# Kernel optimization log

Hardware: AMD Instinct MI355X
Metric: run time of the kernel (lower is better)

## Reference

```python
import jax, jax.numpy as jnp
import numpy as np

TEMPERATURE = 0.1
NORMALIZE = True


def setup_inputs() -> dict:
    key = jax.random.key(0)
    k1, k2 = jax.random.split(key)
    B, D = 4096, 512
    return {
        "z_i": jax.random.normal(k1, (B, D), dtype=jnp.float32),
        "z_j": jax.random.normal(k2, (B, D), dtype=jnp.float32),
    }


def _l2norm(x):
    return x / jnp.sqrt(jnp.sum(x * x, axis=-1, keepdims=True))


def reference(z_i, z_j):
    if NORMALIZE:
        z_i = _l2norm(z_i)
        z_j = _l2norm(z_j)
    B = z_i.shape[0]

    inv_t = 1.0 / TEMPERATURE
    logits_aa = (z_i @ z_i.T) * inv_t  # [B, B]
    logits_bb = (z_j @ z_j.T) * inv_t
    logits_ab = (z_i @ z_j.T) * inv_t
    logits_ba = (z_j @ z_i.T) * inv_t

    # Static off-diagonal column indices: row i keeps cols 0..B-1 except i,
    # in ascending order (matches torch boolean-mask row-major extraction).
    j = jnp.arange(B - 1)[None, :]
    i = jnp.arange(B)[:, None]
    idx = j + (j >= i)  # [B, B-1] int32

    take = lambda m: jnp.take_along_axis(m, idx, axis=1)  # [B, B-1]

    pos = jnp.concatenate([jnp.diagonal(logits_ab), jnp.diagonal(logits_ba)])[:, None]  # [2B, 1]
    neg_a = jnp.concatenate([take(logits_aa), take(logits_ab)], axis=1)  # [B, 2(B-1)]
    neg_b = jnp.concatenate([take(logits_ba), take(logits_bb)], axis=1)
    neg = jnp.concatenate([neg_a, neg_b], axis=0)  # [2B, 2(B-1)]

    logits = jnp.concatenate([pos, neg], axis=1)  # [2B, 2B-1]
    logp = jax.nn.log_softmax(logits, axis=1)
    # Original forward uses labels = torch.ones(2B).long() -> target class 1.
    loss = -jnp.mean(logp[:, 1])
    return loss
```

## Files before the change

### kernel.cpp

```cpp
#include <hip/hip_runtime.h>
#include <hip/hip_bf16.h>
#include <hip/hip_fp8.h>


#define BB 4096
#define DD 512
#define NN 8192
#define TILE 128
#define KB 64
#define NBLK 2080

typedef __attribute__((ext_vector_type(4))) float f32x4;

#define AS1 __attribute__((address_space(1)))
#define AS3 __attribute__((address_space(3)))
static __device__ __forceinline__ void gload_lds16(const void* g, void* l) {
    __builtin_amdgcn_global_load_lds((const AS1 void*)g, (AS3 void*)l, 16, 0, 0);
}

__global__ __launch_bounds__(256)
void normalize_kernel(const float* __restrict__ zi, const float* __restrict__ zj,
                      unsigned char* __restrict__ M, float* __restrict__ rowsum) {
    const int wave = threadIdx.x >> 6;
    const int lane = threadIdx.x & 63;
    const int row  = blockIdx.x * 4 + wave;
    if (threadIdx.x < 4) rowsum[blockIdx.x * 4 + threadIdx.x] = 0.f;
    const float* src = (row < BB) ? (zi + (size_t)row * DD)
                                  : (zj + (size_t)(row - BB) * DD);
    float4 v0 = ((const float4*)src)[lane * 2 + 0];
    float4 v1 = ((const float4*)src)[lane * 2 + 1];
    float ss = v0.x*v0.x + v0.y*v0.y + v0.z*v0.z + v0.w*v0.w
             + v1.x*v1.x + v1.y*v1.y + v1.z*v1.z + v1.w*v1.w;
    #pragma unroll
    for (int off = 1; off <= 32; off <<= 1) ss += __shfl_xor(ss, off);
    const float inv = rsqrtf(ss);
    const float vals[8] = {v0.x*inv, v0.y*inv, v0.z*inv, v0.w*inv,
                           v1.x*inv, v1.y*inv, v1.z*inv, v1.w*inv};
    union { long u; unsigned char b[8]; } pk;
    #pragma unroll
    for (int j = 0; j < 8; ++j)
        pk.b[j] = __hip_cvt_float_to_fp8(vals[j], __HIP_SATFINITE, __HIP_E4M3);
    ((long*)(M + (size_t)row * DD))[lane] = pk.u;
}

__global__ __launch_bounds__(256, 4)
void gram_lse_kernel(const unsigned char* __restrict__ Mg,
                     float* __restrict__ rowsum, float* __restrict__ targets) {
    __shared__ __align__(16) char As[2][TILE * KB];
    __shared__ __align__(16) char Bs[2][TILE * KB];

    const int d = blockIdx.x;
    const int p = (d & 7) * 260 + (d >> 3);
    int by = (int)((sqrtf(8.0f * (float)p + 1.0f) - 1.0f) * 0.5f);
    while ((by + 1) * (by + 2) / 2 <= p) ++by;
    while (by * (by + 1) / 2 > p) --by;
    const int bx = p - by * (by + 1) / 2;

    const int rowBase = bx * TILE;
    const int colBase = by * TILE;
    const bool diag = (bx == by);
    const int tid  = threadIdx.x;
    const int wave = tid >> 6;
    const int lane = tid & 63;
    const int wr = (wave >> 1) * 64;
    const int wc = (wave & 1) * 64;
    const int l15 = lane & 15;
    const int l4  = lane >> 4;

    const int sg  = (tid & 3) ^ ((tid >> 3) & 3);
    const int sr0 = tid >> 2;
    const unsigned char* gA0 = Mg + (size_t)(rowBase + sr0) * DD + sg * 16;
    const unsigned char* gB0 = Mg + (size_t)(colBase + sr0) * DD + sg * 16;

    const int r2 = (l15 >> 1) & 3;
    const int qh = l4 >> 1, ql = l4 & 1;
    const int aoff0 = (wr + l15) * KB + ql * 8;
    const int boff0 = (wc + l15) * KB + ql * 8;

    f32x4 acc[4][4] = {};

    {
        char* lA = As[0] + tid * 16;
        #pragma unroll
        for (int i = 0; i < 2; ++i)
            gload_lds16(gA0 + (size_t)i * 64 * DD, lA + i * 4096);
        if (!diag) {
            char* lB = Bs[0] + tid * 16;
            #pragma unroll
            for (int i = 0; i < 2; ++i)
                gload_lds16(gB0 + (size_t)i * 64 * DD, lB + i * 4096);
        }
    }

    #pragma unroll
    for (int t = 0; t < DD / KB; ++t) {
        __syncthreads();
        if (t < DD / KB - 1) {
            const int k0 = (t + 1) * KB;
            char* lA = As[(t + 1) & 1] + tid * 16;
            #pragma unroll
            for (int i = 0; i < 2; ++i)
                gload_lds16(gA0 + k0 + (size_t)i * 64 * DD, lA + i * 4096);
            if (!diag) {
                char* lB = Bs[(t + 1) & 1] + tid * 16;
                #pragma unroll
                for (int i = 0; i < 2; ++i)
                    gload_lds16(gB0 + k0 + (size_t)i * 64 * DD, lB + i * 4096);
            }
        }
        const char* Asrc = As[t & 1];
        const char* Bsrc = diag ? Asrc : Bs[t & 1];
        #pragma unroll
        for (int ks = 0; ks < 2; ++ks) {
            const int so = ((((ks << 1) | qh) ^ r2) << 4);
            long a[4], b[4];
            #pragma unroll
            for (int mi = 0; mi < 4; ++mi)
                a[mi] = *(const long*)(Asrc + aoff0 + mi * 1024 + so);
            #pragma unroll
            for (int ni = 0; ni < 4; ++ni)
                b[ni] = *(const long*)(Bsrc + boff0 + ni * 1024 + so);
            #pragma unroll
            for (int mi = 0; mi < 4; ++mi)
                #pragma unroll
                for (int ni = 0; ni < 4; ++ni)
                    acc[mi][ni] = __builtin_amdgcn_mfma_f32_16x16x32_fp8_fp8(
                        a[mi], b[ni], acc[mi][ni], 0, 0, 0);
        }
    }

    const float C10 = 14.42695040888963f;
    float cs[4] = {0.f, 0.f, 0.f, 0.f};
    #pragma unroll
    for (int mi = 0; mi < 4; ++mi) {
        float rs[4] = {0.f, 0.f, 0.f, 0.f};
        #pragma unroll
        for (int ni = 0; ni < 4; ++ni) {
            const int gcol = colBase + wc + ni * 16 + l15;
            #pragma unroll
            for (int r = 0; r < 4; ++r) {
                const int grow = rowBase + wr + mi * 16 + l4 * 4 + r;
                float e = __builtin_amdgcn_exp2f(fmaf(acc[mi][ni][r], C10, -C10));
                if (grow == gcol) e = 0.f;
                rs[r] += e;
                cs[ni] += e;
                if (rowBase == 0 && grow < 2) {
                    const int j0 = ((gcol & (BB - 1)) == 0) ? 1 : 0;
                    if (grow == j0) targets[gcol] = 10.f * acc[mi][ni][r];
                }
            }
        }
        #pragma unroll
        for (int m = 1; m <= 8; m <<= 1)
            #pragma unroll
            for (int r = 0; r < 4; ++r)
                rs[r] += __shfl_xor(rs[r], m);
        if (l15 == 0) {
            #pragma unroll
            for (int r = 0; r < 4; ++r)
                atomicAdd(&rowsum[rowBase + wr + mi * 16 + l4 * 4 + r], rs[r]);
        }
    }
    if (!diag) {
        #pragma unroll
        for (int ni = 0; ni < 4; ++ni) {
            cs[ni] += __shfl_xor(cs[ni], 16);
            cs[ni] += __shfl_xor(cs[ni], 32);
        }
        if (l4 == 0) {
            #pragma unroll
            for (int ni = 0; ni < 4; ++ni)
                atomicAdd(&rowsum[colBase + wc + ni * 16 + l15], cs[ni]);
        }
    }
}

__global__ __launch_bounds__(1024)
void finalize_kernel(const float* __restrict__ rowsum,
                     const float* __restrict__ targets, float* __restrict__ out) {
    const int tid = threadIdx.x;
    float s = 0.f;
    #pragma unroll
    for (int t = tid; t < NN; t += 1024)
        s += targets[t] - 10.f - __logf(rowsum[t]);
    #pragma unroll
    for (int off = 1; off <= 32; off <<= 1) s += __shfl_xor(s, off);
    __shared__ float red[16];
    if ((tid & 63) == 0) red[tid >> 6] = s;
    __syncthreads();
    if (tid == 0) {
        float t = 0.f;
        #pragma unroll
        for (int i = 0; i < 16; ++i) t += red[i];
        out[0] = -t / (float)NN;
    }
}

extern "C" void kernel_launch(void* const* d_in, const int* in_sizes, int n_in,
                              void* d_out, int out_size, void* d_ws, size_t ws_size,
                              hipStream_t stream) {
    const float* zi = (const float*)d_in[0];
    const float* zj = (const float*)d_in[1];

    unsigned char* M = (unsigned char*)d_ws;
    float* rowsum  = (float*)((char*)d_ws + (size_t)NN * DD);
    float* targets = rowsum + NN;
    float* out = (float*)d_out;

    normalize_kernel<<<NN / 4, 256, 0, stream>>>(zi, zj, M, rowsum);
    gram_lse_kernel<<<NBLK, 256, 0, stream>>>(M, rowsum, targets);
    finalize_kernel<<<1, 1024, 0, stream>>>(rowsum, targets, out);
}
```

Baseline: 102.9 us.

## Switch gram GEMM to 32x32x64 scaled fp8 MFMA with wider LDS reads

```diff
diff --git a/kernel.cpp b/kernel.cpp
--- a/kernel.cpp
+++ b/kernel.cpp
@@ -10,7 +10,10 @@
 #define KB 64
 #define NBLK 2080
 
-typedef __attribute__((ext_vector_type(4))) float f32x4;
+typedef __attribute__((ext_vector_type(4)))  float f32x4;
+typedef __attribute__((ext_vector_type(16))) float f32x16;
+typedef __attribute__((ext_vector_type(4)))  int   i32x4;
+typedef __attribute__((ext_vector_type(8)))  int   i32x8;
 
 #define AS1 __attribute__((address_space(1)))
 #define AS3 __attribute__((address_space(3)))
@@ -64,20 +67,23 @@
     const int lane = tid & 63;
     const int wr = (wave >> 1) * 64;
     const int wc = (wave & 1) * 64;
-    const int l15 = lane & 15;
-    const int l4  = lane >> 4;
+    const int l31 = lane & 31;
+    const int h0  = lane >> 5;
 
     const int sg  = (tid & 3) ^ ((tid >> 3) & 3);
     const int sr0 = tid >> 2;
     const unsigned char* gA0 = Mg + (size_t)(rowBase + sr0) * DD + sg * 16;
     const unsigned char* gB0 = Mg + (size_t)(colBase + sr0) * DD + sg * 16;
 
-    const int r2 = (l15 >> 1) & 3;
-    const int qh = l4 >> 1, ql = l4 & 1;
-    const int aoff0 = (wr + l15) * KB + ql * 8;
-    const int boff0 = (wc + l15) * KB + ql * 8;
-
-    f32x4 acc[4][4] = {};
+    const int sw  = (l31 >> 1) & 3;
+    const int plo = (2 * h0) ^ sw;
+    const int phi = plo ^ 1;
+    const int aoffL = (wr + l31) * KB + plo * 16;
+    const int aoffH = (wr + l31) * KB + phi * 16;
+    const int boffL = (wc + l31) * KB + plo * 16;
+    const int boffH = (wc + l31) * KB + phi * 16;
+
+    f32x16 acc[2][2] = {};
 
     {
         char* lA = As[0] + tid * 16;
@@ -110,36 +116,40 @@
         }
         const char* Asrc = As[t & 1];
         const char* Bsrc = diag ? Asrc : Bs[t & 1];
-        #pragma unroll
-        for (int ks = 0; ks < 2; ++ks) {
-            const int so = ((((ks << 1) | qh) ^ r2) << 4);
-            long a[4], b[4];
-            #pragma unroll
-            for (int mi = 0; mi < 4; ++mi)
-                a[mi] = *(const long*)(Asrc + aoff0 + mi * 1024 + so);
-            #pragma unroll
-            for (int ni = 0; ni < 4; ++ni)
-                b[ni] = *(const long*)(Bsrc + boff0 + ni * 1024 + so);
-            #pragma unroll
-            for (int mi = 0; mi < 4; ++mi)
-                #pragma unroll
-                for (int ni = 0; ni < 4; ++ni)
-                    acc[mi][ni] = __builtin_amdgcn_mfma_f32_16x16x32_fp8_fp8(
-                        a[mi], b[ni], acc[mi][ni], 0, 0, 0);
-        }
+        i32x8 a[2], b[2];
+        #pragma unroll
+        for (int mi = 0; mi < 2; ++mi) {
+            i32x4 lo = *(const i32x4*)(Asrc + aoffL + mi * 2048);
+            i32x4 hi = *(const i32x4*)(Asrc + aoffH + mi * 2048);
+            a[mi] = __builtin_shufflevector(lo, hi, 0, 1, 2, 3, 4, 5, 6, 7);
+        }
+        #pragma unroll
+        for (int ni = 0; ni < 2; ++ni) {
+            i32x4 lo = *(const i32x4*)(Bsrc + boffL + ni * 2048);
+            i32x4 hi = *(const i32x4*)(Bsrc + boffH + ni * 2048);
+            b[ni] = __builtin_shufflevector(lo, hi, 0, 1, 2, 3, 4, 5, 6, 7);
+        }
+        #pragma unroll
+        for (int mi = 0; mi < 2; ++mi)
+            #pragma unroll
+            for (int ni = 0; ni < 2; ++ni)
+                acc[mi][ni] = __builtin_amdgcn_mfma_scale_f32_32x32x64_f8f6f4(
+                    a[mi], b[ni], acc[mi][ni], 0, 0,
+                    0, 0x7F7F7F7F, 0, 0x7F7F7F7F);
     }
 
     const float C10 = 14.42695040888963f;
-    float cs[4] = {0.f, 0.f, 0.f, 0.f};
-    #pragma unroll
-    for (int mi = 0; mi < 4; ++mi) {
-        float rs[4] = {0.f, 0.f, 0.f, 0.f};
-        #pragma unroll
-        for (int ni = 0; ni < 4; ++ni) {
-            const int gcol = colBase + wc + ni * 16 + l15;
-            #pragma unroll
-            for (int r = 0; r < 4; ++r) {
-                const int grow = rowBase + wr + mi * 16 + l4 * 4 + r;
+    float cs[2] = {0.f, 0.f};
+    #pragma unroll
+    for (int mi = 0; mi < 2; ++mi) {
+        float rs[16] = {};
+        #pragma unroll
+        for (int ni = 0; ni < 2; ++ni) {
+            const int gcol = colBase + wc + ni * 32 + l31;
+            #pragma unroll
+            for (int r = 0; r < 16; ++r) {
+                const int lrow = (r & 3) + 8 * (r >> 2) + 4 * h0;
+                const int grow = rowBase + wr + mi * 32 + lrow;
                 float e = __builtin_amdgcn_exp2f(fmaf(acc[mi][ni][r], C10, -C10));
                 if (grow == gcol) e = 0.f;
                 rs[r] += e;
@@ -151,26 +161,25 @@
             }
         }
         #pragma unroll
-        for (int m = 1; m <= 8; m <<= 1)
-            #pragma unroll
-            for (int r = 0; r < 4; ++r)
+        for (int m = 1; m <= 16; m <<= 1)
+            #pragma unroll
+            for (int r = 0; r < 16; ++r)
                 rs[r] += __shfl_xor(rs[r], m);
-        if (l15 == 0) {
-            #pragma unroll
-            for (int r = 0; r < 4; ++r)
-                atomicAdd(&rowsum[rowBase + wr + mi * 16 + l4 * 4 + r], rs[r]);
+        if (l31 == 0) {
+            #pragma unroll
+            for (int r = 0; r < 16; ++r)
+                atomicAdd(&rowsum[rowBase + wr + mi * 32
+                                  + (r & 3) + 8 * (r >> 2) + 4 * h0], rs[r]);
         }
     }
     if (!diag) {
         #pragma unroll
-        for (int ni = 0; ni < 4; ++ni) {
-            cs[ni] += __shfl_xor(cs[ni], 16);
+        for (int ni = 0; ni < 2; ++ni)
             cs[ni] += __shfl_xor(cs[ni], 32);
-        }
-        if (l4 == 0) {
-            #pragma unroll
-            for (int ni = 0; ni < 4; ++ni)
-                atomicAdd(&rowsum[colBase + wc + ni * 16 + l15], cs[ni]);
+        if (h0 == 0) {
+            #pragma unroll
+            for (int ni = 0; ni < 2; ++ni)
+                atomicAdd(&rowsum[colBase + wc + ni * 32 + l31], cs[ni]);
         }
     }
 }
```

After: 112.3 us. 1.09x slower.

## Triple-buffer gram tiles and replace rowsum atomics with partial-slice reduction

Applied to the files above, without the earlier changes.

```diff
diff --git a/kernel.cpp b/kernel.cpp
--- a/kernel.cpp
+++ b/kernel.cpp
@@ -9,6 +9,7 @@
 #define TILE 128
 #define KB 64
 #define NBLK 2080
+#define NSLICE 256
 
 typedef __attribute__((ext_vector_type(4))) float f32x4;
 
@@ -20,11 +21,11 @@
 
 __global__ __launch_bounds__(256)
 void normalize_kernel(const float* __restrict__ zi, const float* __restrict__ zj,
-                      unsigned char* __restrict__ M, float* __restrict__ rowsum) {
+                      unsigned char* __restrict__ M, float* __restrict__ wacc) {
+    if (blockIdx.x == 0 && threadIdx.x == 0) wacc[0] = 0.f;
     const int wave = threadIdx.x >> 6;
     const int lane = threadIdx.x & 63;
     const int row  = blockIdx.x * 4 + wave;
-    if (threadIdx.x < 4) rowsum[blockIdx.x * 4 + threadIdx.x] = 0.f;
     const float* src = (row < BB) ? (zi + (size_t)row * DD)
                                   : (zj + (size_t)(row - BB) * DD);
     float4 v0 = ((const float4*)src)[lane * 2 + 0];
@@ -43,11 +44,11 @@
     ((long*)(M + (size_t)row * DD))[lane] = pk.u;
 }
 
-__global__ __launch_bounds__(256, 4)
+__global__ __launch_bounds__(256, 3)
 void gram_lse_kernel(const unsigned char* __restrict__ Mg,
-                     float* __restrict__ rowsum, float* __restrict__ targets) {
-    __shared__ __align__(16) char As[2][TILE * KB];
-    __shared__ __align__(16) char Bs[2][TILE * KB];
+                     float* __restrict__ rpart, float* __restrict__ targets) {
+    __shared__ __align__(16) char As[3][TILE * KB];
+    __shared__ __align__(16) char Bs[3][TILE * KB];
 
     const int d = blockIdx.x;
     const int p = (d & 7) * 260 + (d >> 3);
@@ -79,37 +80,28 @@
 
     f32x4 acc[4][4] = {};
 
-    {
-        char* lA = As[0] + tid * 16;
-        #pragma unroll
-        for (int i = 0; i < 2; ++i)
-            gload_lds16(gA0 + (size_t)i * 64 * DD, lA + i * 4096);
-        if (!diag) {
-            char* lB = Bs[0] + tid * 16;
-            #pragma unroll
-            for (int i = 0; i < 2; ++i)
-                gload_lds16(gB0 + (size_t)i * 64 * DD, lB + i * 4096);
-        }
-    }
-
-    #pragma unroll
-    for (int t = 0; t < DD / KB; ++t) {
-        __syncthreads();
-        if (t < DD / KB - 1) {
-            const int k0 = (t + 1) * KB;
-            char* lA = As[(t + 1) & 1] + tid * 16;
-            #pragma unroll
-            for (int i = 0; i < 2; ++i)
-                gload_lds16(gA0 + k0 + (size_t)i * 64 * DD, lA + i * 4096);
-            if (!diag) {
-                char* lB = Bs[(t + 1) & 1] + tid * 16;
-                #pragma unroll
-                for (int i = 0; i < 2; ++i)
-                    gload_lds16(gB0 + k0 + (size_t)i * 64 * DD, lB + i * 4096);
-            }
-        }
-        const char* Asrc = As[t & 1];
-        const char* Bsrc = diag ? Asrc : Bs[t & 1];
+#define STAGE(c) do {                                                   \
+        const int k0_ = (c) * KB;                                       \
+        char* lA_ = As[(c) % 3] + tid * 16;                             \
+        char* lB_ = Bs[(c) % 3] + tid * 16;                             \
+        gload_lds16(gA0 + k0_,           lA_);                          \
+        gload_lds16(gA0 + k0_ + 64 * DD, lA_ + 4096);                   \
+        gload_lds16(gB0 + k0_,           lB_);                          \
+        gload_lds16(gB0 + k0_ + 64 * DD, lB_ + 4096);                   \
+    } while (0)
+
+    STAGE(0);
+    STAGE(1);
+
+    #pragma unroll
+    for (int t = 0; t < 8; ++t) {
+        if (t < 7) asm volatile("s_waitcnt vmcnt(4)" ::: "memory");
+        else       asm volatile("s_waitcnt vmcnt(0)" ::: "memory");
+        __builtin_amdgcn_s_barrier();
+        __builtin_amdgcn_sched_barrier(0);
+        if (t + 2 < 8) STAGE(t + 2);
+        const char* Asrc = As[t % 3];
+        const char* Bsrc = Bs[t % 3];
         #pragma unroll
         for (int ks = 0; ks < 2; ++ks) {
             const int so = ((((ks << 1) | qh) ^ r2) << 4);
@@ -128,6 +120,7 @@
                         a[mi], b[ni], acc[mi][ni], 0, 0, 0);
         }
     }
+#undef STAGE
 
     const float C10 = 14.42695040888963f;
     float cs[4] = {0.f, 0.f, 0.f, 0.f};
@@ -141,7 +134,7 @@
             for (int r = 0; r < 4; ++r) {
                 const int grow = rowBase + wr + mi * 16 + l4 * 4 + r;
                 float e = __builtin_amdgcn_exp2f(fmaf(acc[mi][ni][r], C10, -C10));
-                if (grow == gcol) e = 0.f;
+                if (diag && grow == gcol) e = 0.f;
                 rs[r] += e;
                 cs[ni] += e;
                 if (rowBase == 0 && grow < 2) {
@@ -158,7 +151,8 @@
         if (l15 == 0) {
             #pragma unroll
             for (int r = 0; r < 4; ++r)
-                atomicAdd(&rowsum[rowBase + wr + mi * 16 + l4 * 4 + r], rs[r]);
+                rpart[(size_t)(2 * by + (wave & 1)) * NN
+                      + rowBase + wr + mi * 16 + l4 * 4 + r] = rs[r];
         }
     }
     if (!diag) {
@@ -170,30 +164,37 @@
         if (l4 == 0) {
             #pragma unroll
             for (int ni = 0; ni < 4; ++ni)
-                atomicAdd(&rowsum[colBase + wc + ni * 16 + l15], cs[ni]);
+                rpart[(size_t)(128 + 2 * bx + (wave >> 1)) * NN
+                      + colBase + wc + ni * 16 + l15] = cs[ni];
         }
     }
 }
 
-__global__ __launch_bounds__(1024)
-void finalize_kernel(const float* __restrict__ rowsum,
-                     const float* __restrict__ targets, float* __restrict__ out) {
-    const int tid = threadIdx.x;
+__global__ __launch_bounds__(256)
+void reduce_kernel(const float* __restrict__ rpart,
+                   const float* __restrict__ targets, float* __restrict__ wacc) {
+    const int i = blockIdx.x * 256 + threadIdx.x;
+    const int pi = i >> 7;
     float s = 0.f;
-    #pragma unroll
-    for (int t = tid; t < NN; t += 1024)
-        s += targets[t] - 10.f - __logf(rowsum[t]);
-    #pragma unroll
-    for (int off = 1; off <= 32; off <<= 1) s += __shfl_xor(s, off);
-    __shared__ float red[16];
-    if ((tid & 63) == 0) red[tid >> 6] = s;
+    #pragma unroll 4
+    for (int sl = 2 * pi; sl < 128; ++sl)
+        s += rpart[(size_t)sl * NN + i];
+    #pragma unroll 4
+    for (int sl = 128; sl < 128 + 2 * pi; ++sl)
+        s += rpart[(size_t)sl * NN + i];
+    float term = targets[i] - 10.f - __logf(s);
+    #pragma unroll
+    for (int off = 1; off <= 32; off <<= 1) term += __shfl_xor(term, off);
+    __shared__ float red[4];
+    if ((threadIdx.x & 63) == 0) red[threadIdx.x >> 6] = term;
     __syncthreads();
-    if (tid == 0) {
-        float t = 0.f;
-        #pragma unroll
-        for (int i = 0; i < 16; ++i) t += red[i];
-        out[0] = -t / (float)NN;
-    }
+    if (threadIdx.x == 0)
+        atomicAdd(wacc, red[0] + red[1] + red[2] + red[3]);
+}
+
+__global__ void write_kernel(const float* __restrict__ wacc,
+                             float* __restrict__ out) {
+    out[0] = -wacc[0] / (float)NN;
 }
 
 extern "C" void kernel_launch(void* const* d_in, const int* in_sizes, int n_in,
@@ -203,11 +204,13 @@
     const float* zj = (const float*)d_in[1];
 
     unsigned char* M = (unsigned char*)d_ws;
-    float* rowsum  = (float*)((char*)d_ws + (size_t)NN * DD);
-    float* targets = rowsum + NN;
+    float* rpart   = (float*)((char*)d_ws + (size_t)NN * DD);
+    float* targets = rpart + (size_t)NSLICE * NN;
+    float* wacc    = targets + NN;
     float* out = (float*)d_out;
 
-    normalize_kernel<<<NN / 4, 256, 0, stream>>>(zi, zj, M, rowsum);
-    gram_lse_kernel<<<NBLK, 256, 0, stream>>>(M, rowsum, targets);
-    finalize_kernel<<<1, 1024, 0, stream>>>(rowsum, targets, out);
-}
+    normalize_kernel<<<NN / 4, 256, 0, stream>>>(zi, zj, M, wacc);
+    gram_lse_kernel<<<NBLK, 256, 0, stream>>>(M, rpart, targets);
+    reduce_kernel<<<NN / 256, 256, 0, stream>>>(rpart, targets, wacc);
+    write_kernel<<<1, 1, 0, stream>>>(wacc, out);
+}
```

Result: slower. 114.9 us (+11.6%).
